# Performance work log

Hardware: AMD Instinct MI355X
Metric: run time of the kernel (lower is better)

The kernel has to match this reference:

```python
import jax, jax.numpy as jnp
import numpy as np

B = 512
LIN = 96
LOUT = 96
NUM = 64      # numeric feature size (also decoder output size)
EMB = 32      # embedding dim
HID = 256     # GRU hidden size
VOCAB = 512
IN_SIZE = NUM + EMB


def setup_inputs() -> dict:
    key = jax.random.key(0)
    ks = jax.random.split(key, 9)
    s = 0.05
    return {
        "input_num": jax.random.normal(ks[0], (B, LIN + LOUT, NUM), dtype=jnp.float32),
        "input_cat": jax.random.randint(ks[1], (B, LIN + LOUT), 0, VOCAB),
        "emb_table": jax.random.normal(ks[2], (VOCAB, EMB), dtype=jnp.float32) * s,
        "W_ih": jax.random.normal(ks[3], (3 * HID, IN_SIZE), dtype=jnp.float32) * s,
        "W_hh": jax.random.normal(ks[4], (3 * HID, HID), dtype=jnp.float32) * s,
        "b_ih": jax.random.normal(ks[5], (3 * HID,), dtype=jnp.float32) * s,
        "b_hh": jax.random.normal(ks[6], (3 * HID,), dtype=jnp.float32) * s,
        "W_dec": jax.random.normal(ks[7], (NUM, HID), dtype=jnp.float32) * s,
        "b_dec": jax.random.normal(ks[8], (NUM,), dtype=jnp.float32) * s,
    }


def _gru_step(h, x, W_ih, W_hh, b_ih, b_hh):
    # PyTorch GRU cell math. h: [B,H], x: [B,in]
    H = h.shape[-1]
    gx = x @ W_ih.T + b_ih   # [B, 3H]
    gh = h @ W_hh.T + b_hh   # [B, 3H]
    r = jax.nn.sigmoid(gx[:, :H] + gh[:, :H])
    z = jax.nn.sigmoid(gx[:, H:2 * H] + gh[:, H:2 * H])
    n = jnp.tanh(gx[:, 2 * H:] + r * gh[:, 2 * H:])
    return (1.0 - z) * n + z * h


def reference(input_num, input_cat, emb_table, W_ih, W_hh, b_ih, b_hh, W_dec, b_dec):
    emb_seq = emb_table[input_cat]                      # [B, T, EMB]
    # ---- encoder over first LIN steps ----
    enc_in = jnp.concatenate([input_num[:, :LIN], emb_seq[:, :LIN]], axis=-1)
    h0 = jnp.zeros((input_num.shape[0], HID), dtype=input_num.dtype)

    def enc_body(h, x_t):
        return _gru_step(h, x_t, W_ih, W_hh, b_ih, b_hh), None

    h, _ = jax.lax.scan(enc_body, h0, jnp.swapaxes(enc_in, 0, 1))
    # single-layer GRU: output at last step == hidden state
    out0 = h @ W_dec.T + b_dec                          # [B, NUM]

    dec_emb = jnp.swapaxes(emb_seq[:, LIN:LIN + LOUT - 1], 0, 1)  # [LOUT-1, B, EMB]

    def dec_body(carry, e_t):
        h, out_prev = carry
        x = jnp.concatenate([out_prev, e_t], axis=-1)
        h_new = _gru_step(h, x, W_ih, W_hh, b_ih, b_hh)
        out = h_new @ W_dec.T + b_dec
        return (h_new, out), out

    _, outs = jax.lax.scan(dec_body, (h, out0), dec_emb)  # [LOUT-1, B, NUM]
    return jnp.concatenate([out0[:, None], jnp.swapaxes(outs, 0, 1)], axis=1)  # [B, LOUT, NUM]
```

## Files before the change

kernel.cpp:

```cpp
#include <hip/hip_runtime.h>


#define BATCH 512
#define TSEQ  192
#define LIN_  96
#define LOUT_ 96
#define NUM_  64
#define EMB_  32
#define HID_  256
#define INS_  96

#define NBLK  32
#define NT    512
#define XSTR  360

#define WS_WL   0u
#define WS_WS   98304u
#define WS_WD   245760u
#define WS_NEED 278528u

typedef __attribute__((ext_vector_type(8))) short short8_t;
typedef __attribute__((ext_vector_type(4))) float float4_t;
typedef unsigned short us;

__device__ __forceinline__ us f2bf(float x) {
    unsigned u = __builtin_bit_cast(unsigned, x);
    u = (u + 0x7FFFu + ((u >> 16) & 1u)) >> 16;
    return (us)u;
}
__device__ __forceinline__ float sigm(float x) {
    return __builtin_amdgcn_rcpf(1.0f + __builtin_amdgcn_exp2f(-1.44269504f * x));
}
__device__ __forceinline__ float tanhx(float x) {
    return 2.0f * __builtin_amdgcn_rcpf(1.0f + __builtin_amdgcn_exp2f(-2.88539008f * x)) - 1.0f;
}

__device__ __forceinline__ void bar_lds() {
    __builtin_amdgcn_sched_barrier(0);
    asm volatile("s_waitcnt lgkmcnt(0)" ::: "memory");
    __builtin_amdgcn_s_barrier();
    __builtin_amdgcn_sched_barrier(0);
}

__device__ __forceinline__ short8_t pack8(const float* v) {
    short8_t s;
    #pragma unroll
    for (int j = 0; j < 8; ++j) s[j] = (short)f2bf(v[j]);
    return s;
}

#define MFMA16(a, b, c) __builtin_amdgcn_mfma_f32_16x16x32_bf16((a), (b), (c), 0, 0, 0)

__global__ void prep_v11(const float* __restrict__ W_hh, const float* __restrict__ W_dec,
                         unsigned char* __restrict__ ws) {
    us* WLi = (us*)(ws + WS_WL);
    us* WSi = (us*)(ws + WS_WS);
    us* WDi = (us*)(ws + WS_WD);
    const int idx = blockIdx.x * 256 + threadIdx.x;
    if (idx >= 272 * 64) return;
    const int f = idx >> 6, l = idx & 63;
    const int r16 = l & 15, kq8 = (l >> 4) * 8;
    float tmp[8];
    if (f < 96) {
        const int g = f >> 5, rem = f & 31, tt = rem >> 1, cs = rem & 1;
        const int grow = g * 256 + tt * 16 + r16;
        const int k = (6 + cs) * 32 + kq8;
        #pragma unroll
        for (int j = 0; j < 8; ++j) tmp[j] = W_hh[(size_t)grow * HID_ + (k - INS_) + j];
        *(short8_t*)(WLi + (size_t)f * 512 + l * 8) = pack8(tmp);
    } else if (f < 240) {
        const int s = f - 96, g = s / 48, rem = s % 48, tt = rem / 3, cs = rem % 3;
        const int grow = g * 256 + tt * 16 + r16;
        const int k = (8 + cs) * 32 + kq8;
        #pragma unroll
        for (int j = 0; j < 8; ++j) tmp[j] = W_hh[(size_t)grow * HID_ + (k - INS_) + j];
        *(short8_t*)(WSi + (size_t)s * 512 + l * 8) = pack8(tmp);
    } else {
        const int f3 = f - 240, tt = f3 >> 3, c = f3 & 7;
        const int urow = tt * 16 + r16, k = c * 32 + kq8;
        #pragma unroll
        for (int j = 0; j < 8; ++j) tmp[j] = W_dec[(size_t)urow * HID_ + k + j];
        *(short8_t*)(WDi + (size_t)f3 * 512 + l * 8) = pack8(tmp);
    }
}

__global__ __launch_bounds__(NT, 2) void gru_v11(
    const float* __restrict__ input_num, const int* __restrict__ input_cat,
    const float* __restrict__ emb_table,
    const float* __restrict__ W_ih, const float* __restrict__ W_hh,
    const float* __restrict__ b_ih, const float* __restrict__ b_hh,
    const float* __restrict__ b_dec,
    const unsigned char* __restrict__ ws, float* __restrict__ out)
{
    __shared__ __align__(16) us XH[16 * XSTR];
    __shared__ __align__(16) us WLl[96 * 512];
    __shared__ __align__(16) us WDl[32 * 512];

    const us* WSf = (const us*)(ws + WS_WS);

    const int t = threadIdx.x, wave = t >> 6, lane = t & 63;
    const int arow = lane & 15, quad = lane >> 4, kq = quad * 8;
    const int bb = blockIdx.x * 16;
    const int tt0 = 2 * wave, tt1 = 2 * wave + 1;

    short8_t wfr[2][3][6];
    #pragma unroll
    for (int ti = 0; ti < 2; ++ti) {
        #pragma unroll
        for (int g3 = 0; g3 < 3; ++g3) {
            const int grow = g3 * HID_ + 32 * wave + 16 * ti + arow;
            #pragma unroll
            for (int kc = 0; kc < 6; ++kc) {
                float tmp[8];
                #pragma unroll
                for (int j2 = 0; j2 < 2; ++j2) {
                    const int k = kc * 32 + kq + j2 * 4;
                    float4 v = (k < INS_)
                        ? *(const float4*)&W_ih[(size_t)grow * INS_ + k]
                        : *(const float4*)&W_hh[(size_t)grow * HID_ + (k - INS_)];
                    tmp[j2 * 4 + 0] = v.x; tmp[j2 * 4 + 1] = v.y;
                    tmp[j2 * 4 + 2] = v.z; tmp[j2 * 4 + 3] = v.w;
                }
                wfr[ti][g3][kc] = pack8(tmp);
            }
        }
    }

    {
        const us* WLi = (const us*)(ws + WS_WL);
        const us* WDi = (const us*)(ws + WS_WD);
        for (int c = t; c < 96 * 64; c += NT)
            *(ulonglong2*)&WLl[c * 8] = *(const ulonglong2*)&WLi[c * 8];
        for (int c = t; c < 32 * 64; c += NT)
            *(ulonglong2*)&WDl[c * 8] = *(const ulonglong2*)&WDi[c * 8];
        for (int c = t; c < 16 * XSTR; c += NT) XH[c] = 0;
    }

    float bRr[2], bZr[2], bNXr[2], bNHr[2];
    #pragma unroll
    for (int ti = 0; ti < 2; ++ti) {
        const int u = 32 * wave + 16 * ti + arow;
        bRr[ti]  = b_ih[u] + b_hh[u];
        bZr[ti]  = b_ih[HID_ + u] + b_hh[HID_ + u];
        bNXr[ti] = b_ih[2 * HID_ + u];
        bNHr[ti] = b_hh[2 * HID_ + u];
    }
    const float bdr = (wave < 4) ? b_dec[wave * 16 + arow] : 0.0f;
    float hr[2][4] = {{0.f,0.f,0.f,0.f},{0.f,0.f,0.f,0.f}};

    const int srow = t >> 4, sq = t & 15;
    const int erow = (t - 256) >> 3, eq = (t - 256) & 7;
    const bool isN = (t < 256), isE = (t >= 256 && t < 384);
    float4 pnum = {0.f,0.f,0.f,0.f}, pemb = {0.f,0.f,0.f,0.f};
    int pcat = 0;
    if (isN) {
        pnum = *(const float4*)&input_num[((size_t)(bb + srow) * TSEQ + 0) * NUM_ + sq * 4];
    } else if (isE) {
        const int c0 = input_cat[(bb + erow) * TSEQ + 0];
        pemb = *(const float4*)&emb_table[(size_t)c0 * EMB_ + eq * 4];
        pcat = input_cat[(bb + erow) * TSEQ + 1];
    }
    __syncthreads();

    for (int sg = 1; sg <= 191; ++sg) {
        if (sg <= 96) {
            if (isN) {
                ushort4 s = { f2bf(pnum.x), f2bf(pnum.y), f2bf(pnum.z), f2bf(pnum.w) };
                *(ushort4*)&XH[srow * XSTR + sq * 4] = s;
            } else if (isE) {
                ushort4 s = { f2bf(pemb.x), f2bf(pemb.y), f2bf(pemb.z), f2bf(pemb.w) };
                *(ushort4*)&XH[erow * XSTR + NUM_ + eq * 4] = s;
            }
        } else if (isE) {
            ushort4 s = { f2bf(pemb.x), f2bf(pemb.y), f2bf(pemb.z), f2bf(pemb.w) };
            *(ushort4*)&XH[erow * XSTR + NUM_ + eq * 4] = s;
        }
        if (isN && sg <= 95)
            pnum = *(const float4*)&input_num[((size_t)(bb + srow) * TSEQ + sg) * NUM_ + sq * 4];
        if (isE && sg <= 190) {
            pemb = *(const float4*)&emb_table[(size_t)pcat * EMB_ + eq * 4];
            if (sg <= 189) pcat = input_cat[(bb + erow) * TSEQ + sg + 1];
        }
        bar_lds();

        if (sg > 96) {
            if (wave < 4) {
                float4_t acc = {0.f, 0.f, 0.f, 0.f};
                #pragma unroll
                for (int c = 0; c < 8; ++c) {
                    short8_t b = *(const short8_t*)&WDl[(wave * 8 + c) * 512 + lane * 8];
                    short8_t a = *(const short8_t*)&XH[arow * XSTR + INS_ + c * 32 + kq];
                    acc = MFMA16(a, b, acc);
                }
                const int cg = wave * 16 + arow, pos = sg - 97;
                #pragma unroll
                for (int i = 0; i < 4; ++i) {
                    const int row = quad * 4 + i;
                    const float val = acc[i] + bdr;
                    XH[row * XSTR + cg] = f2bf(val);
                    out[((size_t)(bb + row) * LOUT_ + pos) * NUM_ + cg] = val;
                }
            }
            bar_lds();
        }

        float4_t aR[2]  = {{0.f,0.f,0.f,0.f},{0.f,0.f,0.f,0.f}};
        float4_t aZ[2]  = {{0.f,0.f,0.f,0.f},{0.f,0.f,0.f,0.f}};
        float4_t aNX[2] = {{0.f,0.f,0.f,0.f},{0.f,0.f,0.f,0.f}};
        float4_t aNH[2] = {{0.f,0.f,0.f,0.f},{0.f,0.f,0.f,0.f}};

        short8_t s8[6], s9[6];
        #pragma unroll
        for (int g = 0; g < 3; ++g) {
            s8[g * 2 + 0] = *(const short8_t*)&WSf[(size_t)(g * 48 + tt0 * 3 + 0) * 512 + lane * 8];
            s8[g * 2 + 1] = *(const short8_t*)&WSf[(size_t)(g * 48 + tt1 * 3 + 0) * 512 + lane * 8];
            s9[g * 2 + 0] = *(const short8_t*)&WSf[(size_t)(g * 48 + tt0 * 3 + 1) * 512 + lane * 8];
            s9[g * 2 + 1] = *(const short8_t*)&WSf[(size_t)(g * 48 + tt1 * 3 + 1) * 512 + lane * 8];
        }

        #pragma unroll
        for (int kc = 0; kc < 6; ++kc) {
            short8_t a = *(const short8_t*)&XH[arow * XSTR + kc * 32 + kq];
            #pragma unroll
            for (int ti = 0; ti < 2; ++ti) {
                aR[ti] = MFMA16(a, wfr[ti][0][kc], aR[ti]);
                aZ[ti] = MFMA16(a, wfr[ti][1][kc], aZ[ti]);
                if (kc < 3) aNX[ti] = MFMA16(a, wfr[ti][2][kc], aNX[ti]);
                else        aNH[ti] = MFMA16(a, wfr[ti][2][kc], aNH[ti]);
            }
        }
        #pragma unroll
        for (int cs = 0; cs < 2; ++cs) {
            short8_t a = *(const short8_t*)&XH[arow * XSTR + (6 + cs) * 32 + kq];
            #pragma unroll
            for (int ti = 0; ti < 2; ++ti) {
                const int tt = tt0 + ti;
                short8_t b0 = *(const short8_t*)&WLl[(0 * 32 + tt * 2 + cs) * 512 + lane * 8];
                short8_t b1 = *(const short8_t*)&WLl[(1 * 32 + tt * 2 + cs) * 512 + lane * 8];
                short8_t b2 = *(const short8_t*)&WLl[(2 * 32 + tt * 2 + cs) * 512 + lane * 8];
                aR[ti] = MFMA16(a, b0, aR[ti]);
                aZ[ti] = MFMA16(a, b1, aZ[ti]);
                aNH[ti] = MFMA16(a, b2, aNH[ti]);
            }
        }
        short8_t s10[6];
        #pragma unroll
        for (int g = 0; g < 3; ++g) {
            s10[g * 2 + 0] = *(const short8_t*)&WSf[(size_t)(g * 48 + tt0 * 3 + 2) * 512 + lane * 8];
            s10[g * 2 + 1] = *(const short8_t*)&WSf[(size_t)(g * 48 + tt1 * 3 + 2) * 512 + lane * 8];
        }
        {
            short8_t a = *(const short8_t*)&XH[arow * XSTR + 8 * 32 + kq];
            #pragma unroll
            for (int ti = 0; ti < 2; ++ti) {
                aR[ti] = MFMA16(a, s8[0 * 2 + ti], aR[ti]);
                aZ[ti] = MFMA16(a, s8[1 * 2 + ti], aZ[ti]);
                aNH[ti] = MFMA16(a, s8[2 * 2 + ti], aNH[ti]);
            }
            a = *(const short8_t*)&XH[arow * XSTR + 9 * 32 + kq];
            #pragma unroll
            for (int ti = 0; ti < 2; ++ti) {
                aR[ti] = MFMA16(a, s9[0 * 2 + ti], aR[ti]);
                aZ[ti] = MFMA16(a, s9[1 * 2 + ti], aZ[ti]);
                aNH[ti] = MFMA16(a, s9[2 * 2 + ti], aNH[ti]);
            }
            a = *(const short8_t*)&XH[arow * XSTR + 10 * 32 + kq];
            #pragma unroll
            for (int ti = 0; ti < 2; ++ti) {
                aR[ti] = MFMA16(a, s10[0 * 2 + ti], aR[ti]);
                aZ[ti] = MFMA16(a, s10[1 * 2 + ti], aZ[ti]);
                aNH[ti] = MFMA16(a, s10[2 * 2 + ti], aNH[ti]);
            }
        }

        #pragma unroll
        for (int ti = 0; ti < 2; ++ti) {
            #pragma unroll
            for (int i = 0; i < 4; ++i) {
                const float r = sigm(aR[ti][i] + bRr[ti]);
                const float z = sigm(aZ[ti][i] + bZr[ti]);
                const float n = tanhx(aNX[ti][i] + bNXr[ti] + r * (aNH[ti][i] + bNHr[ti]));
                hr[ti][i] = (1.0f - z) * n + z * hr[ti][i];
            }
        }

        bar_lds();
        #pragma unroll
        for (int ti = 0; ti < 2; ++ti) {
            #pragma unroll
            for (int i = 0; i < 4; ++i)
                XH[(quad * 4 + i) * XSTR + INS_ + 32 * wave + 16 * ti + arow] = f2bf(hr[ti][i]);
        }
    }

    bar_lds();
    if (wave < 4) {
        float4_t acc = {0.f, 0.f, 0.f, 0.f};
        #pragma unroll
        for (int c = 0; c < 8; ++c) {
            short8_t b = *(const short8_t*)&WDl[(wave * 8 + c) * 512 + lane * 8];
            short8_t a = *(const short8_t*)&XH[arow * XSTR + INS_ + c * 32 + kq];
            acc = MFMA16(a, b, acc);
        }
        const int cg = wave * 16 + arow;
        #pragma unroll
        for (int i = 0; i < 4; ++i) {
            const int row = quad * 4 + i;
            out[((size_t)(bb + row) * LOUT_ + 95) * NUM_ + cg] = acc[i] + bdr;
        }
    }
}

__global__ __launch_bounds__(512) void gru_fallback(
    const float* __restrict__ input_num, const int* __restrict__ input_cat,
    const float* __restrict__ emb_table,
    const float* __restrict__ W_ih, const float* __restrict__ W_hh,
    const float* __restrict__ b_ih, const float* __restrict__ b_hh,
    const float* __restrict__ W_dec, const float* __restrict__ b_dec,
    float* __restrict__ out)
{
    __shared__ __align__(16) float xh[4][352];
    __shared__ float wdec[NUM_ * 257];
    const int t = threadIdx.x, bbase = blockIdx.x * 4;
    const int u = t & 255, rb = (t >> 8) * 2;
    for (int i = t; i < NUM_ * HID_; i += 512) wdec[(i >> 8) * 257 + (i & 255)] = W_dec[i];
    for (int i = t; i < 4 * HID_; i += 512) xh[i >> 8][INS_ + (i & 255)] = 0.0f;
    const float bR = b_ih[u] + b_hh[u], bZ = b_ih[256 + u] + b_hh[256 + u];
    const float bNX = b_ih[512 + u], bNH = b_hh[512 + u], bD = b_dec[t & 63];
    __syncthreads();
    auto sg_ = [](float x) { return 1.0f / (1.0f + __expf(-x)); };
    auto th_ = [](float x) { return 2.0f / (1.0f + __expf(-2.0f * x)) - 1.0f; };
    auto step = [&]() {
        float aR0 = bR, aR1 = bR, aZ0 = bZ, aZ1 = bZ, aNX0 = bNX, aNX1 = bNX, aNH0 = bNH, aNH1 = bNH;
        const float* x0 = xh[rb]; const float* x1 = xh[rb + 1];
        for (int kb = 0; kb < 88; ++kb) {
            float4 w0, w1, w2; int k4 = kb * 4;
            if (k4 < INS_) {
                w0 = *(const float4*)&W_ih[(size_t)u * INS_ + k4];
                w1 = *(const float4*)&W_ih[(size_t)(256 + u) * INS_ + k4];
                w2 = *(const float4*)&W_ih[(size_t)(512 + u) * INS_ + k4];
            } else {
                int kh = k4 - INS_;
                w0 = *(const float4*)&W_hh[(size_t)u * HID_ + kh];
                w1 = *(const float4*)&W_hh[(size_t)(256 + u) * HID_ + kh];
                w2 = *(const float4*)&W_hh[(size_t)(512 + u) * HID_ + kh];
            }
            float4 a = *(const float4*)&x0[k4], c = *(const float4*)&x1[k4];
            aR0 += w0.x*a.x+w0.y*a.y+w0.z*a.z+w0.w*a.w; aR1 += w0.x*c.x+w0.y*c.y+w0.z*c.z+w0.w*c.w;
            aZ0 += w1.x*a.x+w1.y*a.y+w1.z*a.z+w1.w*a.w; aZ1 += w1.x*c.x+w1.y*c.y+w1.z*c.z+w1.w*c.w;
            if (k4 < INS_) { aNX0 += w2.x*a.x+w2.y*a.y+w2.z*a.z+w2.w*a.w; aNX1 += w2.x*c.x+w2.y*c.y+w2.z*c.z+w2.w*c.w; }
            else           { aNH0 += w2.x*a.x+w2.y*a.y+w2.z*a.z+w2.w*a.w; aNH1 += w2.x*c.x+w2.y*c.y+w2.z*c.z+w2.w*c.w; }
        }
        float h0 = x0[INS_ + u], h1 = x1[INS_ + u];
        __syncthreads();
        { float r = sg_(aR0), z = sg_(aZ0), n = th_(aNX0 + r * aNH0);
          xh[rb][INS_ + u] = (1 - z) * n + z * h0; }
        { float r = sg_(aR1), z = sg_(aZ1), n = th_(aNX1 + r * aNH1);
          xh[rb + 1][INS_ + u] = (1 - z) * n + z * h1; }
        __syncthreads();
    };
    auto project = [&](int pos) {
        if (t < 256) {
            int r = t >> 6, m = t & 63;
            const float* wr = &wdec[m * 257]; const float* hr2 = &xh[r][INS_];
            float acc = bD;
            for (int k = 0; k < HID_; ++k) acc = fmaf(wr[k], hr2[k], acc);
            out[((size_t)(bbase + r) * LOUT_ + pos) * NUM_ + m] = acc;
            xh[r][m] = acc;
        }
    };
    for (int s = 0; s < LIN_; ++s) {
        if (t < 256) { int r = t >> 6, k = t & 63;
            xh[r][k] = input_num[((size_t)(bbase + r) * TSEQ + s) * NUM_ + k]; }
        if (t < 128) { int r = t >> 5, e = t & 31;
            xh[r][NUM_ + e] = emb_table[input_cat[(bbase + r) * TSEQ + s] * EMB_ + e]; }
        __syncthreads();
        step();
    }
    project(0);
    for (int s = 0; s < LOUT_ - 1; ++s) {
        if (t < 128) { int r = t >> 5, e = t & 31;
            xh[r][NUM_ + e] = emb_table[input_cat[(bbase + r) * TSEQ + LIN_ + s] * EMB_ + e]; }
        __syncthreads();
        step();
        project(s + 1);
    }
}

extern "C" void kernel_launch(void* const* d_in, const int* in_sizes, int n_in,
                              void* d_out, int out_size, void* d_ws, size_t ws_size,
                              hipStream_t stream) {
    const float* input_num = (const float*)d_in[0];
    const int*   input_cat = (const int*)d_in[1];
    const float* emb_table = (const float*)d_in[2];
    const float* W_ih      = (const float*)d_in[3];
    const float* W_hh      = (const float*)d_in[4];
    const float* b_ih      = (const float*)d_in[5];
    const float* b_hh      = (const float*)d_in[6];
    const float* W_dec     = (const float*)d_in[7];
    const float* b_dec     = (const float*)d_in[8];
    float* out = (float*)d_out;

    if (ws_size >= WS_NEED) {
        unsigned char* ws = (unsigned char*)d_ws;
        prep_v11<<<68, 256, 0, stream>>>(W_hh, W_dec, ws);
        gru_v11<<<NBLK, NT, 0, stream>>>(input_num, input_cat, emb_table,
                                         W_ih, W_hh, b_ih, b_hh, b_dec, ws, out);
    } else {
        gru_fallback<<<BATCH / 4, 512, 0, stream>>>(input_num, input_cat, emb_table,
                                                    W_ih, W_hh, b_ih, b_hh, W_dec, b_dec, out);
    }
}
```

Measured before the change: 1.019 ms.

## Double-buffer hidden and input LDS tiles to cut per-step barriers

The single XH staging buffer becomes ping-pong buffers for the hidden state, numeric input and embedding input. The hidden-state write and the staging of the next step's inputs now happen before one trailing barrier, replacing the earlier pre-step, post-decoder and pre-write barriers. In decoder steps the hidden-part MFMAs run before the decoder-output barrier, so only the numeric-input MFMAs wait on it. Streamed-weight addresses are also precomputed as wave-uniform offsets. The cost is a larger LDS footprint and more intricate buffer-index bookkeeping.

```diff
diff --git a/kernel.cpp b/kernel.cpp
--- a/kernel.cpp
+++ b/kernel.cpp
@@ -12,7 +12,9 @@
 
 #define NBLK  32
 #define NT    512
-#define XSTR  360
+#define XSTR  712
+#define XEMB0 128
+#define XHB   192
 
 #define WS_WL   0u
 #define WS_WS   98304u
@@ -51,7 +53,7 @@
 
 #define MFMA16(a, b, c) __builtin_amdgcn_mfma_f32_16x16x32_bf16((a), (b), (c), 0, 0, 0)
 
-__global__ void prep_v11(const float* __restrict__ W_hh, const float* __restrict__ W_dec,
+__global__ void prep_v12(const float* __restrict__ W_hh, const float* __restrict__ W_dec,
                          unsigned char* __restrict__ ws) {
     us* WLi = (us*)(ws + WS_WL);
     us* WSi = (us*)(ws + WS_WS);
@@ -84,7 +86,7 @@
     }
 }
 
-__global__ __launch_bounds__(NT, 2) void gru_v11(
+__global__ __launch_bounds__(NT, 2) void gru_v12(
     const float* __restrict__ input_num, const int* __restrict__ input_cat,
     const float* __restrict__ emb_table,
     const float* __restrict__ W_ih, const float* __restrict__ W_hh,
@@ -148,90 +150,90 @@
     const float bdr = (wave < 4) ? b_dec[wave * 16 + arow] : 0.0f;
     float hr[2][4] = {{0.f,0.f,0.f,0.f},{0.f,0.f,0.f,0.f}};
 
+    unsigned sbase[6];
+    #pragma unroll
+    for (int g = 0; g < 3; ++g) {
+        sbase[g * 2 + 0] = __builtin_amdgcn_readfirstlane((unsigned)((g * 48 + tt0 * 3) * 1024));
+        sbase[g * 2 + 1] = __builtin_amdgcn_readfirstlane((unsigned)((g * 48 + tt1 * 3) * 1024));
+    }
+    const char* WSbase = (const char*)WSf + (size_t)lane * 16;
+
     const int srow = t >> 4, sq = t & 15;
     const int erow = (t - 256) >> 3, eq = (t - 256) & 7;
     const bool isN = (t < 256), isE = (t >= 256 && t < 384);
     float4 pnum = {0.f,0.f,0.f,0.f}, pemb = {0.f,0.f,0.f,0.f};
     int pcat = 0;
     if (isN) {
-        pnum = *(const float4*)&input_num[((size_t)(bb + srow) * TSEQ + 0) * NUM_ + sq * 4];
+        float4 v = *(const float4*)&input_num[((size_t)(bb + srow) * TSEQ + 0) * NUM_ + sq * 4];
+        ushort4 s = { f2bf(v.x), f2bf(v.y), f2bf(v.z), f2bf(v.w) };
+        *(ushort4*)&XH[srow * XSTR + sq * 4] = s;
+        pnum = *(const float4*)&input_num[((size_t)(bb + srow) * TSEQ + 1) * NUM_ + sq * 4];
     } else if (isE) {
         const int c0 = input_cat[(bb + erow) * TSEQ + 0];
-        pemb = *(const float4*)&emb_table[(size_t)c0 * EMB_ + eq * 4];
-        pcat = input_cat[(bb + erow) * TSEQ + 1];
+        float4 v = *(const float4*)&emb_table[(size_t)c0 * EMB_ + eq * 4];
+        ushort4 s = { f2bf(v.x), f2bf(v.y), f2bf(v.z), f2bf(v.w) };
+        *(ushort4*)&XH[erow * XSTR + XEMB0 + eq * 4] = s;
+        const int c1 = input_cat[(bb + erow) * TSEQ + 1];
+        pemb = *(const float4*)&emb_table[(size_t)c1 * EMB_ + eq * 4];
+        pcat = input_cat[(bb + erow) * TSEQ + 2];
     }
     __syncthreads();
 
     for (int sg = 1; sg <= 191; ++sg) {
-        if (sg <= 96) {
-            if (isN) {
-                ushort4 s = { f2bf(pnum.x), f2bf(pnum.y), f2bf(pnum.z), f2bf(pnum.w) };
-                *(ushort4*)&XH[srow * XSTR + sq * 4] = s;
-            } else if (isE) {
-                ushort4 s = { f2bf(pemb.x), f2bf(pemb.y), f2bf(pemb.z), f2bf(pemb.w) };
-                *(ushort4*)&XH[erow * XSTR + NUM_ + eq * 4] = s;
-            }
-        } else if (isE) {
-            ushort4 s = { f2bf(pemb.x), f2bf(pemb.y), f2bf(pemb.z), f2bf(pemb.w) };
-            *(ushort4*)&XH[erow * XSTR + NUM_ + eq * 4] = s;
-        }
-        if (isN && sg <= 95)
-            pnum = *(const float4*)&input_num[((size_t)(bb + srow) * TSEQ + sg) * NUM_ + sq * 4];
-        if (isE && sg <= 190) {
-            pemb = *(const float4*)&emb_table[(size_t)pcat * EMB_ + eq * 4];
-            if (sg <= 189) pcat = input_cat[(bb + erow) * TSEQ + sg + 1];
-        }
-        bar_lds();
-
-        if (sg > 96) {
-            if (wave < 4) {
-                float4_t acc = {0.f, 0.f, 0.f, 0.f};
-                #pragma unroll
-                for (int c = 0; c < 8; ++c) {
-                    short8_t b = *(const short8_t*)&WDl[(wave * 8 + c) * 512 + lane * 8];
-                    short8_t a = *(const short8_t*)&XH[arow * XSTR + INS_ + c * 32 + kq];
-                    acc = MFMA16(a, b, acc);
-                }
-                const int cg = wave * 16 + arow, pos = sg - 97;
-                #pragma unroll
-                for (int i = 0; i < 4; ++i) {
-                    const int row = quad * 4 + i;
-                    const float val = acc[i] + bdr;
-                    XH[row * XSTR + cg] = f2bf(val);
-                    out[((size_t)(bb + row) * LOUT_ + pos) * NUM_ + cg] = val;
-                }
-            }
-            bar_lds();
+        const int bx = (sg - 1) & 1, hn = sg & 1;
+        const int hb = XHB + bx * 256;
+
+        short8_t s8[6], s9[6];
+        #pragma unroll
+        for (int i = 0; i < 6; ++i) {
+            s8[i] = *(const short8_t*)(WSbase + sbase[i]);
+            s9[i] = *(const short8_t*)(WSbase + sbase[i] + 1024);
+        }
+
+        if (sg > 96 && wave < 4) {
+            float4_t acc = {0.f, 0.f, 0.f, 0.f};
+            #pragma unroll
+            for (int c = 0; c < 8; ++c) {
+                short8_t b = *(const short8_t*)&WDl[(wave * 8 + c) * 512 + lane * 8];
+                short8_t a = *(const short8_t*)&XH[arow * XSTR + hb + c * 32 + kq];
+                acc = MFMA16(a, b, acc);
+            }
+            const int cg = wave * 16 + arow, pos = sg - 97;
+            #pragma unroll
+            for (int i = 0; i < 4; ++i) {
+                const int row = quad * 4 + i;
+                const float val = acc[i] + bdr;
+                XH[row * XSTR + bx * 64 + cg] = f2bf(val);
+                out[((size_t)(bb + row) * LOUT_ + pos) * NUM_ + cg] = val;
+            }
         }
 
         float4_t aR[2]  = {{0.f,0.f,0.f,0.f},{0.f,0.f,0.f,0.f}};
         float4_t aZ[2]  = {{0.f,0.f,0.f,0.f},{0.f,0.f,0.f,0.f}};
         float4_t aNX[2] = {{0.f,0.f,0.f,0.f},{0.f,0.f,0.f,0.f}};
         float4_t aNH[2] = {{0.f,0.f,0.f,0.f},{0.f,0.f,0.f,0.f}};
-
-        short8_t s8[6], s9[6];
-        #pragma unroll
-        for (int g = 0; g < 3; ++g) {
-            s8[g * 2 + 0] = *(const short8_t*)&WSf[(size_t)(g * 48 + tt0 * 3 + 0) * 512 + lane * 8];
-            s8[g * 2 + 1] = *(const short8_t*)&WSf[(size_t)(g * 48 + tt1 * 3 + 0) * 512 + lane * 8];
-            s9[g * 2 + 0] = *(const short8_t*)&WSf[(size_t)(g * 48 + tt0 * 3 + 1) * 512 + lane * 8];
-            s9[g * 2 + 1] = *(const short8_t*)&WSf[(size_t)(g * 48 + tt1 * 3 + 1) * 512 + lane * 8];
-        }
-
-        #pragma unroll
-        for (int kc = 0; kc < 6; ++kc) {
-            short8_t a = *(const short8_t*)&XH[arow * XSTR + kc * 32 + kq];
+        short8_t a;
+
+        a = *(const short8_t*)&XH[arow * XSTR + XEMB0 + bx * 32 + kq];
+        #pragma unroll
+        for (int ti = 0; ti < 2; ++ti) {
+            aR[ti] = MFMA16(a, wfr[ti][0][2], aR[ti]);
+            aZ[ti] = MFMA16(a, wfr[ti][1][2], aZ[ti]);
+            aNX[ti] = MFMA16(a, wfr[ti][2][2], aNX[ti]);
+        }
+        #pragma unroll
+        for (int kc = 3; kc < 6; ++kc) {
+            a = *(const short8_t*)&XH[arow * XSTR + hb + (kc - 3) * 32 + kq];
             #pragma unroll
             for (int ti = 0; ti < 2; ++ti) {
                 aR[ti] = MFMA16(a, wfr[ti][0][kc], aR[ti]);
                 aZ[ti] = MFMA16(a, wfr[ti][1][kc], aZ[ti]);
-                if (kc < 3) aNX[ti] = MFMA16(a, wfr[ti][2][kc], aNX[ti]);
-                else        aNH[ti] = MFMA16(a, wfr[ti][2][kc], aNH[ti]);
+                aNH[ti] = MFMA16(a, wfr[ti][2][kc], aNH[ti]);
             }
         }
         #pragma unroll
         for (int cs = 0; cs < 2; ++cs) {
-            short8_t a = *(const short8_t*)&XH[arow * XSTR + (6 + cs) * 32 + kq];
+            a = *(const short8_t*)&XH[arow * XSTR + hb + (3 + cs) * 32 + kq];
             #pragma unroll
             for (int ti = 0; ti < 2; ++ti) {
                 const int tt = tt0 + ti;
@@ -245,32 +247,45 @@
         }
         short8_t s10[6];
         #pragma unroll
-        for (int g = 0; g < 3; ++g) {
-            s10[g * 2 + 0] = *(const short8_t*)&WSf[(size_t)(g * 48 + tt0 * 3 + 2) * 512 + lane * 8];
-            s10[g * 2 + 1] = *(const short8_t*)&WSf[(size_t)(g * 48 + tt1 * 3 + 2) * 512 + lane * 8];
-        }
-        {
-            short8_t a = *(const short8_t*)&XH[arow * XSTR + 8 * 32 + kq];
-            #pragma unroll
-            for (int ti = 0; ti < 2; ++ti) {
-                aR[ti] = MFMA16(a, s8[0 * 2 + ti], aR[ti]);
-                aZ[ti] = MFMA16(a, s8[1 * 2 + ti], aZ[ti]);
-                aNH[ti] = MFMA16(a, s8[2 * 2 + ti], aNH[ti]);
-            }
-            a = *(const short8_t*)&XH[arow * XSTR + 9 * 32 + kq];
-            #pragma unroll
-            for (int ti = 0; ti < 2; ++ti) {
-                aR[ti] = MFMA16(a, s9[0 * 2 + ti], aR[ti]);
-                aZ[ti] = MFMA16(a, s9[1 * 2 + ti], aZ[ti]);
-                aNH[ti] = MFMA16(a, s9[2 * 2 + ti], aNH[ti]);
-            }
-            a = *(const short8_t*)&XH[arow * XSTR + 10 * 32 + kq];
-            #pragma unroll
-            for (int ti = 0; ti < 2; ++ti) {
-                aR[ti] = MFMA16(a, s10[0 * 2 + ti], aR[ti]);
-                aZ[ti] = MFMA16(a, s10[1 * 2 + ti], aZ[ti]);
-                aNH[ti] = MFMA16(a, s10[2 * 2 + ti], aNH[ti]);
-            }
+        for (int i = 0; i < 6; ++i)
+            s10[i] = *(const short8_t*)(WSbase + sbase[i] + 2048);
+        a = *(const short8_t*)&XH[arow * XSTR + hb + 5 * 32 + kq];
+        #pragma unroll
+        for (int ti = 0; ti < 2; ++ti) {
+            aR[ti] = MFMA16(a, s8[0 * 2 + ti], aR[ti]);
+            aZ[ti] = MFMA16(a, s8[1 * 2 + ti], aZ[ti]);
+            aNH[ti] = MFMA16(a, s8[2 * 2 + ti], aNH[ti]);
+        }
+        a = *(const short8_t*)&XH[arow * XSTR + hb + 6 * 32 + kq];
+        #pragma unroll
+        for (int ti = 0; ti < 2; ++ti) {
+            aR[ti] = MFMA16(a, s9[0 * 2 + ti], aR[ti]);
+            aZ[ti] = MFMA16(a, s9[1 * 2 + ti], aZ[ti]);
+            aNH[ti] = MFMA16(a, s9[2 * 2 + ti], aNH[ti]);
+        }
+        a = *(const short8_t*)&XH[arow * XSTR + hb + 7 * 32 + kq];
+        #pragma unroll
+        for (int ti = 0; ti < 2; ++ti) {
+            aR[ti] = MFMA16(a, s10[0 * 2 + ti], aR[ti]);
+            aZ[ti] = MFMA16(a, s10[1 * 2 + ti], aZ[ti]);
+            aNH[ti] = MFMA16(a, s10[2 * 2 + ti], aNH[ti]);
+        }
+
+        if (sg > 96) bar_lds();
+
+        a = *(const short8_t*)&XH[arow * XSTR + bx * 64 + kq];
+        #pragma unroll
+        for (int ti = 0; ti < 2; ++ti) {
+            aR[ti] = MFMA16(a, wfr[ti][0][0], aR[ti]);
+            aZ[ti] = MFMA16(a, wfr[ti][1][0], aZ[ti]);
+            aNX[ti] = MFMA16(a, wfr[ti][2][0], aNX[ti]);
+        }
+        a = *(const short8_t*)&XH[arow * XSTR + bx * 64 + 32 + kq];
+        #pragma unroll
+        for (int ti = 0; ti < 2; ++ti) {
+            aR[ti] = MFMA16(a, wfr[ti][0][1], aR[ti]);
+            aZ[ti] = MFMA16(a, wfr[ti][1][1], aZ[ti]);
+            aNX[ti] = MFMA16(a, wfr[ti][2][1], aNX[ti]);
         }
 
         #pragma unroll
@@ -284,22 +299,38 @@
             }
         }
 
+        #pragma unroll
+        for (int ti = 0; ti < 2; ++ti) {
+            #pragma unroll
+            for (int i = 0; i < 4; ++i)
+                XH[(quad * 4 + i) * XSTR + XHB + hn * 256 + 32 * wave + 16 * ti + arow] = f2bf(hr[ti][i]);
+        }
+        if (sg <= 190) {
+            if (isN) {
+                if (sg <= 95) {
+                    ushort4 s = { f2bf(pnum.x), f2bf(pnum.y), f2bf(pnum.z), f2bf(pnum.w) };
+                    *(ushort4*)&XH[srow * XSTR + hn * 64 + sq * 4] = s;
+                }
+                if (sg <= 94)
+                    pnum = *(const float4*)&input_num[((size_t)(bb + srow) * TSEQ + sg + 1) * NUM_ + sq * 4];
+            } else if (isE) {
+                ushort4 s = { f2bf(pemb.x), f2bf(pemb.y), f2bf(pemb.z), f2bf(pemb.w) };
+                *(ushort4*)&XH[erow * XSTR + XEMB0 + hn * 32 + eq * 4] = s;
+                if (sg <= 189) {
+                    pemb = *(const float4*)&emb_table[(size_t)pcat * EMB_ + eq * 4];
+                    if (sg <= 188) pcat = input_cat[(bb + erow) * TSEQ + sg + 2];
+                }
+            }
+        }
         bar_lds();
-        #pragma unroll
-        for (int ti = 0; ti < 2; ++ti) {
-            #pragma unroll
-            for (int i = 0; i < 4; ++i)
-                XH[(quad * 4 + i) * XSTR + INS_ + 32 * wave + 16 * ti + arow] = f2bf(hr[ti][i]);
-        }
-    }
-
-    bar_lds();
+    }
+
     if (wave < 4) {
         float4_t acc = {0.f, 0.f, 0.f, 0.f};
         #pragma unroll
         for (int c = 0; c < 8; ++c) {
             short8_t b = *(const short8_t*)&WDl[(wave * 8 + c) * 512 + lane * 8];
-            short8_t a = *(const short8_t*)&XH[arow * XSTR + INS_ + c * 32 + kq];
+            short8_t a = *(const short8_t*)&XH[arow * XSTR + XHB + 256 + c * 32 + kq];
             acc = MFMA16(a, b, acc);
         }
         const int cg = wave * 16 + arow;
@@ -403,8 +434,8 @@
 
     if (ws_size >= WS_NEED) {
         unsigned char* ws = (unsigned char*)d_ws;
-        prep_v11<<<68, 256, 0, stream>>>(W_hh, W_dec, ws);
-        gru_v11<<<NBLK, NT, 0, stream>>>(input_num, input_cat, emb_table,
+        prep_v12<<<68, 256, 0, stream>>>(W_hh, W_dec, ws);
+        gru_v12<<<NBLK, NT, 0, stream>>>(input_num, input_cat, emb_table,
                                          W_ih, W_hh, b_ih, b_hh, b_dec, ws, out);
     } else {
         gru_fallback<<<BATCH / 4, 512, 0, stream>>>(input_num, input_cat, emb_table,
```

Result: slower. 1.179 ms (+15.7%).
